# Performance work log

Measured on AMD Instinct MI355X. Metric: run time of the kernel, lower is better.

## Reference

```python
import jax, jax.numpy as jnp
import numpy as np

B, C, H, W = 16, 512, 64, 64
CB, CG = 64, 256  # bottleneck = C/8, g = C/2


def _conv1x1(x, w, b):
    # x: [B,Cin,H,W], w: [Cout,Cin] -> [B,Cout,H,W]
    return jnp.einsum('bchw,oc->bohw', x, w) + b[None, :, None, None]


def _avg_pool2(x):
    # 2x2 average pool, stride 2. x: [B,C,H,W] with even H,W.
    b, c, h, w = x.shape
    return x.reshape(b, c, h // 2, 2, w // 2, 2).mean(axis=(3, 5))


def setup_inputs() -> dict:
    key = jax.random.key(0)
    ks = jax.random.split(key, 6)
    s = 0.02
    return {
        'x': jax.random.normal(ks[0], (B, C, H, W), jnp.float32),
        'w_theta': jax.random.normal(ks[1], (CB, C), jnp.float32) * s,
        'b_theta': jnp.zeros((CB,), jnp.float32),
        'w_phi': jax.random.normal(ks[2], (CB, C), jnp.float32) * s,
        'b_phi': jnp.zeros((CB,), jnp.float32),
        'w_g': jax.random.normal(ks[3], (CG, C), jnp.float32) * s,
        'b_g': jnp.zeros((CG,), jnp.float32),
        'w_out': jax.random.normal(ks[4], (C, CG), jnp.float32) * s,
        'b_out': jnp.zeros((C,), jnp.float32),
        'gamma': jnp.zeros((1,), jnp.float32),
    }


def reference(x, w_theta, b_theta, w_phi, b_phi, w_g, b_g, w_out, b_out, gamma):
    b, c, h, w = x.shape
    n = h * w          # query locations
    m = n // 4         # pooled key/value locations

    theta = _conv1x1(x, w_theta, b_theta).reshape(b, CB, n)           # [B,CB,N]
    phi = _avg_pool2(_conv1x1(x, w_phi, b_phi)).reshape(b, CB, m)     # [B,CB,M]
    g = _avg_pool2(_conv1x1(x, w_g, b_g)).reshape(b, CG, m)           # [B,CG,M]

    logits = jnp.einsum('bcn,bcm->bnm', theta, phi)                   # [B,N,M]
    attn = jax.nn.softmax(logits, axis=-1)
    out = jnp.einsum('bcm,bnm->bcn', g, attn).reshape(b, CG, h, w)    # [B,CG,H,W]
    out = _conv1x1(out, w_out, b_out)                                 # [B,C,H,W]
    return gamma[0] * out + x
```

## Files before the change

### kernel.cpp

```cpp
#include <hip/hip_runtime.h>
#include <math.h>


typedef unsigned short u16;
typedef short bf16x8 __attribute__((ext_vector_type(8)));
typedef float f32x16 __attribute__((ext_vector_type(16)));
typedef u16 u16x4 __attribute__((ext_vector_type(4)));
typedef int i32x4 __attribute__((ext_vector_type(4)));

#define MFMA32 __builtin_amdgcn_mfma_f32_32x32x16_bf16
#define B_ 16
#define C_ 512
#define N_ 4096
#define M_ 1024
#define LOG2E 1.44269504088896f
#define FIXMAX 8.0f

__device__ __forceinline__ u16 f2b(float f) {
  unsigned u = __float_as_uint(f);
  return (u16)((u + 0x7FFFu + ((u >> 16) & 1u)) >> 16);
}
__device__ __forceinline__ unsigned cvtpk(float a, float b) {
  unsigned r;
  asm("v_cvt_pk_bf16_f32 %0, %1, %2" : "=v"(r) : "v"(a), "v"(b));
  return r;
}
__device__ __forceinline__ void permswap(unsigned &a, unsigned &b) {
  asm("v_permlane32_swap_b32 %0, %1" : "+v"(a), "+v"(b));
}
__device__ __forceinline__ float exp2v(float a) {
  float r;
  asm("v_exp_f32 %0, %1" : "=v"(r) : "v"(a));
  return r;
}
__device__ __forceinline__ void async_cp16(u16* lds, const u16* g) {
  __builtin_amdgcn_global_load_lds(
      (const __attribute__((address_space(1))) unsigned int*)g,
      (__attribute__((address_space(3))) unsigned int*)lds, 16, 0, 0);
}
__device__ __forceinline__ f32x16 fz16() {
  f32x16 z;
#pragma unroll
  for (int i = 0; i < 16; ++i) z[i] = 0.0f;
  return z;
}


__global__ __launch_bounds__(256) void cvt_all_kernel(
    const float* __restrict__ w_theta, const float* __restrict__ w_phi,
    const float* __restrict__ w_g, const float* __restrict__ w_out,
    const float* __restrict__ gamma, u16* __restrict__ dth, u16* __restrict__ dph,
    u16* __restrict__ dg, u16* __restrict__ dwo) {
  int i = blockIdx.x * 256 + threadIdx.x;
  if (i < 16384) {
    const float* s = (i < 8192) ? w_theta : w_phi;
    u16* d = (i < 8192) ? dth : dph;
    float scale = (i < 8192) ? LOG2E : 1.0f;
    int j = i & 8191;
    int o = j >> 7, c = (j & 127) * 4;
    float4 vv = *(const float4*)(s + (size_t)o * 512 + c);
    int idx = (((o >> 5) * 8 + (c >> 6)) * 4 + ((c >> 4) & 3)) * 512 +
              (((c >> 3) & 1) * 32 + (o & 31)) * 8 + (c & 7);
    u16x4 ot = {f2b(vv.x * scale), f2b(vv.y * scale), f2b(vv.z * scale), f2b(vv.w * scale)};
    *(u16x4*)(d + idx) = ot;
  } else if (i < 49152) {
    int j = i - 16384;
    int o = j >> 7, c = (j & 127) * 4;
    float4 vv = *(const float4*)(w_g + (size_t)o * 512 + c);
    int idx = (((o >> 5) * 8 + (c >> 6)) * 4 + ((c >> 4) & 3)) * 512 +
              (((c >> 3) & 1) * 32 + (o & 31)) * 8 + (c & 7);
    u16x4 ot = {f2b(vv.x), f2b(vv.y), f2b(vv.z), f2b(vv.w)};
    *(u16x4*)(dg + idx) = ot;
  } else {
    int j = i - 49152;
    int o = j >> 6, k = (j & 63) * 4;
    float scale = gamma[0];
    float4 vv = *(const float4*)(w_out + (size_t)o * 256 + k);
    int idx = ((o >> 5) * 16 + (k >> 4)) * 512 +
              (((k >> 3) & 1) * 32 + (o & 31)) * 8 + (k & 7);
    u16x4 ot = {f2b(vv.x * scale), f2b(vv.y * scale), f2b(vv.z * scale), f2b(vv.w * scale)};
    *(u16x4*)(dwo + idx) = ot;
  }
}

__global__ __launch_bounds__(512) void prep_kernel(
    const float* __restrict__ x, const u16* __restrict__ wth,
    const u16* __restrict__ wph, const u16* __restrict__ wg,
    const float* __restrict__ bth, const float* __restrict__ bph,
    const float* __restrict__ bg, u16* __restrict__ th, u16* __restrict__ ph,
    u16* __restrict__ vt) {
  __shared__ u16 xb[128 * 68];
  __shared__ u16 xpt[32 * 68];
  const int t = threadIdx.x;
  const int w = t >> 6, l = t & 63, lo = l & 31, hi = l >> 5;
  const int nb = blockIdx.x, b = blockIdx.y;
  const int n0 = nb * 128;
  const int lcol = (t & 31) * 4;
  const int lrow = t >> 5;

  f32x16 acc0 = fz16(), acc1 = fz16(), a_ph = fz16();

  float v[16];
  auto loadv = [&](int c0) {
#pragma unroll
    for (int i = 0; i < 4; ++i) {
      float4 f = *(const float4*)(x + ((size_t)(b * C_ + c0 + lrow + 16 * i)) * N_ + n0 + lcol);
      v[4*i] = f.x; v[4*i+1] = f.y; v[4*i+2] = f.z; v[4*i+3] = f.w;
    }
  };
  auto writeT = [&]() {
#pragma unroll
    for (int i = 0; i < 4; ++i) {
      int c = lrow + 16 * i;
      int blk = c >> 3;
#pragma unroll
      for (int k = 0; k < 4; ++k) {
        int n = lcol + k;
        int swz = ((n >> 2) ^ (n >> 5)) & 7;
        xb[n * 68 + ((blk ^ swz) * 8) + (c & 7)] = f2b(v[4*i+k]);
      }
    }
    float pA[4], pB[4];
#pragma unroll
    for (int i = 0; i < 4; ++i) {
      pA[i] = v[4*i] + v[4*i+1];
      pB[i] = v[4*i+2] + v[4*i+3];
    }
#pragma unroll
    for (int i = 0; i < 4; ++i) {
      pA[i] += __shfl_xor(pA[i], 16, 64);
      pB[i] += __shfl_xor(pB[i], 16, 64);
    }
    if ((t & 31) < 16) {
      int m0 = (t & 31) * 2;
#pragma unroll
      for (int i = 0; i < 4; ++i) {
        int c = lrow + 16 * i;
        xpt[m0 * 68 + c] = f2b(0.25f * pA[i]);
        xpt[(m0 + 1) * 68 + c] = f2b(0.25f * pB[i]);
      }
    }
  };
  auto domfma = [&](int c0b) {
    if (w < 4) {
      const int n = 32 * w + lo;
      const int rbase = n * 68;
      const int nswz = ((n >> 2) ^ (n >> 5)) & 7;
#pragma unroll
      for (int kh = 0; kh < 4; ++kh) {
        bf16x8 xa = *(const bf16x8*)(&xb[rbase + (((2*kh + hi) ^ nswz) * 8)]);
        bf16x8 w0 = *(const bf16x8*)(wth + ((c0b) * 4 + kh) * 512 + l * 8);
        bf16x8 w1 = *(const bf16x8*)(wth + ((8 + c0b) * 4 + kh) * 512 + l * 8);
        acc0 = MFMA32(xa, w0, acc0, 0, 0, 0);
        acc1 = MFMA32(xa, w1, acc1, 0, 0, 0);
      }
    } else {
      const int wg4 = w - 4;
      const u16* xpw = &xpt[lo * 68];
#pragma unroll
      for (int kh = 0; kh < 4; ++kh) {
        bf16x8 xp8 = *(const bf16x8*)(xpw + kh * 16 + hi * 8);
        bf16x8 g0 = *(const bf16x8*)(wg + ((16*wg4 + c0b) * 4 + kh) * 512 + l * 8);
        bf16x8 g1 = *(const bf16x8*)(wg + ((16*wg4 + 8 + c0b) * 4 + kh) * 512 + l * 8);
        acc0 = MFMA32(g0, xp8, acc0, 0, 0, 0);
        acc1 = MFMA32(g1, xp8, acc1, 0, 0, 0);
        if (wg4 < 2) {
          bf16x8 wp8 = *(const bf16x8*)(wph + ((wg4*8 + c0b) * 4 + kh) * 512 + l * 8);
          a_ph = MFMA32(xp8, wp8, a_ph, 0, 0, 0);
        }
      }
    }
  };

  loadv(0);
  for (int i = 0; i < 8; ++i) {
    if (i) __syncthreads();
    writeT();
    if (i < 7) loadv((i + 1) * 64);
    __syncthreads();
    domfma(i);
  }

  int rr[16];
#pragma unroll
  for (int r = 0; r < 16; ++r) rr[r] = (r & 3) + 8 * (r >> 2) + 4 * hi;

  if (w < 4) {
    u16* thb = th + (size_t)b * 262144;
#pragma unroll
    for (int r = 0; r < 16; ++r) {
      int sub = (((lo >> 3) & 1) * 32 + rr[r]) * 8 + (lo & 7);
      thb[((nb*4 + w)*4 + (lo >> 4)) * 512 + sub]     = f2b(acc0[r] + LOG2E * bth[lo]);
      thb[((nb*4 + w)*4 + 2 + (lo >> 4)) * 512 + sub] = f2b(acc1[r] + LOG2E * bth[32 + lo]);
    }
  } else {
    const int wg4 = w - 4;
    u16* vtb = vt + (size_t)b * 262144;
#pragma unroll
    for (int r = 0; r < 16; ++r) {
      int cg0 = 64 * wg4 + rr[r];
      int sub = (((lo >> 3) & 1) * 32 + rr[r]) * 8 + (lo & 7);
      int kk = (nb & 1) * 2 + (lo >> 4);
      vtb[(((nb >> 1) * 8 + 2*wg4) * 4 + kk) * 512 + sub]     = f2b(acc0[r] + bg[cg0]);
      vtb[(((nb >> 1) * 8 + 2*wg4 + 1) * 4 + kk) * 512 + sub] = f2b(acc1[r] + bg[cg0 + 32]);
    }
    if (wg4 < 2) {
      u16* phb = ph + (size_t)b * 65536;
#pragma unroll
      for (int r = 0; r < 16; ++r) {
        int sub = (((lo >> 3) & 1) * 32 + rr[r]) * 8 + (lo & 7);
        phb[(nb*4 + 2*wg4 + (lo >> 4)) * 512 + sub] = f2b(a_ph[r] + bph[32*wg4 + lo]);
      }
    }
  }
}

__global__ __launch_bounds__(512, 4) void attn_core_kernel(
    const u16* __restrict__ th, const u16* __restrict__ ph,
    const u16* __restrict__ vt, u16* __restrict__ Og) {
  __shared__ u16 smem[40960];

  const int t = threadIdx.x;
  const int w = t >> 6, l = t & 63;
  const int p = w & 3, h = w >> 2;
  const int flat = blockIdx.y * 32 + blockIdx.x;
  const int nf = (flat & 7) * 64 + (flat >> 3);
  const int b = nf >> 5, nb5 = nf & 31;
  const int jqt = nb5 * 4 + p;

  const u16* thb = th + (size_t)b * 262144;
  const u16* phb = ph + (size_t)b * 65536;
  const u16* vtb = vt + (size_t)b * 262144;

  bf16x8 thB[4];
#pragma unroll
  for (int kh = 0; kh < 4; ++kh)
    thB[kh] = *(const bf16x8*)(thb + (jqt * 4 + kh) * 512 + l * 8);

  f32x16 acc[4];
#pragma unroll
  for (int ct = 0; ct < 4; ++ct) acc[ct] = fz16();
  float sp[4] = {0.0f, 0.0f, 0.0f, 0.0f};

  auto stage = [&](int k) {
    const int ic = k >> 1, jml2 = (k & 1) * 2;
    u16* base = &smem[(k & 3) * 10240];
#pragma unroll
    for (int i = 0; i < 2; ++i) {
      const int r = w + 8 * i;
      const u16* src = vtb + (size_t)((ic * 8 + (r >> 1)) * 4 + jml2 + (r & 1)) * 512 + l * 8;
      async_cp16(base + r * 512 + l * 8, src);
    }
    {
      const int o2 = (t & 255) * 8;
      async_cp16(base + 8192 + o2, phb + (size_t)k * 2048 + o2);
    }
  };

  stage(0);
  stage(1);
  asm volatile("s_waitcnt vmcnt(3)" ::: "memory");
  __builtin_amdgcn_sched_barrier(0);
  __builtin_amdgcn_s_barrier();

  for (int k = 0; k < 32; ++k) {
    if (k < 30) stage(k + 2);

    const u16* Vs = &smem[(k & 3) * 10240];
    const u16* Ps = Vs + 8192;

    f32x16 S = fz16();
#pragma unroll
    for (int kh = 0; kh < 4; ++kh) {
      bf16x8 pf = *(const bf16x8*)(Ps + kh * 512 + l * 8);
      S = MFMA32(pf, thB[kh], S, 0, 0, 0);
    }

#pragma unroll
    for (int i = 0; i < 16; ++i) {
      S[i] = exp2v(S[i] - FIXMAX);
      sp[i & 3] += S[i];
    }

    bf16x8 Pf[2];
#pragma unroll
    for (int s = 0; s < 2; ++s) {
      unsigned a0 = cvtpk(S[8*s+0], S[8*s+1]);
      unsigned a1 = cvtpk(S[8*s+2], S[8*s+3]);
      unsigned a2 = cvtpk(S[8*s+4], S[8*s+5]);
      unsigned a3 = cvtpk(S[8*s+6], S[8*s+7]);
      permswap(a0, a2);
      permswap(a1, a3);
      i32x4 wv = {(int)a0, (int)a1, (int)a2, (int)a3};
      Pf[s] = __builtin_bit_cast(bf16x8, wv);
    }

    __builtin_amdgcn_s_setprio(1);
#pragma unroll
    for (int ct2 = 0; ct2 < 4; ++ct2) {
      const u16* vp = Vs + (4 * h + ct2) * 1024 + l * 8;
      bf16x8 vf0 = *(const bf16x8*)(vp);
      bf16x8 vf1 = *(const bf16x8*)(vp + 512);
      acc[ct2] = MFMA32(vf0, Pf[0], acc[ct2], 0, 0, 0);
      acc[ct2] = MFMA32(vf1, Pf[1], acc[ct2], 0, 0, 0);
    }
    __builtin_amdgcn_s_setprio(0);

    if (k < 30) {
      asm volatile("s_waitcnt vmcnt(3)" ::: "memory");
      __builtin_amdgcn_sched_barrier(0);
      __builtin_amdgcn_s_barrier();
    } else if (k == 30) {
      asm volatile("s_waitcnt vmcnt(0)" ::: "memory");
      __builtin_amdgcn_sched_barrier(0);
      __builtin_amdgcn_s_barrier();
    }
  }

  float lsum = (sp[0] + sp[1]) + (sp[2] + sp[3]);
  lsum += __shfl_xor(lsum, 32, 64);
  const float linv = 1.0f / lsum;

  u16* Ob = Og + (size_t)b * 1048576 + (size_t)jqt * 16 * 512;
#pragma unroll
  for (int ct2 = 0; ct2 < 4; ++ct2) {
    f32x16& A = acc[ct2];
#pragma unroll
    for (int s = 0; s < 2; ++s) {
      unsigned a0 = cvtpk(A[8*s+0]*linv, A[8*s+1]*linv);
      unsigned a1 = cvtpk(A[8*s+2]*linv, A[8*s+3]*linv);
      unsigned a2 = cvtpk(A[8*s+4]*linv, A[8*s+5]*linv);
      unsigned a3 = cvtpk(A[8*s+6]*linv, A[8*s+7]*linv);
      permswap(a0, a2);
      permswap(a1, a3);
      i32x4 wv = {(int)a0, (int)a1, (int)a2, (int)a3};
      int f = 8 * h + 2 * ct2 + s;
      *(bf16x8*)(Ob + f * 512 + l * 8) = __builtin_bit_cast(bf16x8, wv);
    }
  }
}

__global__ __launch_bounds__(512, 4) void outconv_kernel(
    const u16* __restrict__ Og, const u16* __restrict__ wo,
    const float* __restrict__ b_out, const float* __restrict__ gamma,
    const float* __restrict__ x, float* __restrict__ out) {
  const int t = threadIdx.x;
  const int w = t >> 6, l = t & 63, lo = l & 31, hi = l >> 5;
  const int p = w & 3, h = w >> 2;
  const int flat = blockIdx.y * 32 + blockIdx.x;
  const int nf = (flat & 7) * 64 + (flat >> 3);
  const int b = nf >> 5, nb5 = nf & 31;
  const int jqt = nb5 * 4 + p;
  const int qp = jqt * 32;

  const u16* Ob = Og + (size_t)b * 1048576 + (size_t)jqt * 16 * 512;
  bf16x8 Of[16];
#pragma unroll
  for (int f = 0; f < 16; ++f)
    Of[f] = *(const bf16x8*)(Ob + f * 512 + l * 8);

  int rr[16];
#pragma unroll
  for (int r = 0; r < 16; ++r) rr[r] = (r & 3) + 8 * (r >> 2) + 4 * hi;

  const float gamma0 = gamma[0];
  for (int ctc = 0; ctc < 8; ++ctc) {
    f32x16 facc = fz16();
    const u16* wp = wo + (size_t)((8 * h + ctc) * 16) * 512 + l * 8;
#pragma unroll
    for (int f = 0; f < 16; ++f) {
      bf16x8 wfr = *(const bf16x8*)(wp + f * 512);
      facc = MFMA32(wfr, Of[f], facc, 0, 0, 0);
    }
#pragma unroll
    for (int r = 0; r < 16; ++r) {
      int c = 256 * h + 32 * ctc + rr[r];
      size_t idx = ((size_t)(b * C_ + c)) * N_ + qp + lo;
      float xv = __builtin_nontemporal_load(&x[idx]);
      __builtin_nontemporal_store(facc[r] + gamma0 * b_out[c] + xv, &out[idx]);
    }
  }
}

extern "C" void kernel_launch(void* const* d_in, const int* in_sizes, int n_in,
                              void* d_out, int out_size, void* d_ws, size_t ws_size,
                              hipStream_t stream) {
  (void)in_sizes; (void)n_in; (void)out_size; (void)ws_size;
  const float* x       = (const float*)d_in[0];
  const float* w_theta = (const float*)d_in[1];
  const float* b_theta = (const float*)d_in[2];
  const float* w_phi   = (const float*)d_in[3];
  const float* b_phi   = (const float*)d_in[4];
  const float* w_g     = (const float*)d_in[5];
  const float* b_g     = (const float*)d_in[6];
  const float* w_out   = (const float*)d_in[7];
  const float* b_out   = (const float*)d_in[8];
  const float* gamma   = (const float*)d_in[9];
  float* out = (float*)d_out;

  char* ws = (char*)d_ws;
  u16* th  = (u16*)(ws);
  u16* ph  = (u16*)(ws + 8388608);
  u16* vt  = (u16*)(ws + 10485760);
  u16* wth = (u16*)(ws + 18874368);
  u16* wph = (u16*)(ws + 18939904);
  u16* wg  = (u16*)(ws + 19005440);
  u16* wo  = (u16*)(ws + 19267584);
  u16* Og  = (u16*)(ws + 19529728);

  cvt_all_kernel<<<320, 256, 0, stream>>>(w_theta, w_phi, w_g, w_out, gamma,
                                          wth, wph, wg, wo);
  prep_kernel<<<dim3(32, 16), 512, 0, stream>>>(x, wth, wph, wg, b_theta, b_phi,
                                                b_g, th, ph, vt);
  attn_core_kernel<<<dim3(32, 16), 512, 0, stream>>>(th, ph, vt, Og);
  outconv_kernel<<<dim3(32, 16), 512, 0, stream>>>(Og, wo, b_out, gamma, x, out);
}
```

Before: 167.8 us.

## Process two query tiles per wave in attention core to reuse staged K/V

Each wave now handles two 32-query tiles instead of one, so each block covers twice the queries and the grid is halved. The staged phi and V tiles in shared memory, and the phi fragments read from them, are reused across both tiles, which halves global and LDS traffic per query. In exchange, register pressure doubles (two accumulator sets), launch bounds drop to 2 blocks per CU, and the grid has only 256 blocks. The shared memory array is enlarged, though the staging indices still use the old layout.

```diff
diff --git a/kernel.cpp b/kernel.cpp
--- a/kernel.cpp
+++ b/kernel.cpp
@@ -215,32 +215,34 @@
   }
 }
 
-__global__ __launch_bounds__(512, 4) void attn_core_kernel(
+__global__ __launch_bounds__(512, 2) void attn_core_kernel(
     const u16* __restrict__ th, const u16* __restrict__ ph,
     const u16* __restrict__ vt, u16* __restrict__ Og) {
-  __shared__ u16 smem[40960];
+  __shared__ u16 smem[49152];
 
   const int t = threadIdx.x;
   const int w = t >> 6, l = t & 63;
   const int p = w & 3, h = w >> 2;
-  const int flat = blockIdx.y * 32 + blockIdx.x;
-  const int nf = (flat & 7) * 64 + (flat >> 3);
-  const int b = nf >> 5, nb5 = nf & 31;
-  const int jqt = nb5 * 4 + p;
+  const int flat = blockIdx.y * 16 + blockIdx.x;
+  const int nf = (flat & 7) * 32 + (flat >> 3);
+  const int b = nf >> 4, nb6 = nf & 15;
+  const int jA = nb6 * 8 + p * 2, jB = jA + 1;
 
   const u16* thb = th + (size_t)b * 262144;
   const u16* phb = ph + (size_t)b * 65536;
   const u16* vtb = vt + (size_t)b * 262144;
 
-  bf16x8 thB[4];
-#pragma unroll
-  for (int kh = 0; kh < 4; ++kh)
-    thB[kh] = *(const bf16x8*)(thb + (jqt * 4 + kh) * 512 + l * 8);
-
-  f32x16 acc[4];
-#pragma unroll
-  for (int ct = 0; ct < 4; ++ct) acc[ct] = fz16();
-  float sp[4] = {0.0f, 0.0f, 0.0f, 0.0f};
+  bf16x8 thA[4], thBt[4];
+#pragma unroll
+  for (int kh = 0; kh < 4; ++kh) {
+    thA[kh]  = *(const bf16x8*)(thb + (jA * 4 + kh) * 512 + l * 8);
+    thBt[kh] = *(const bf16x8*)(thb + (jB * 4 + kh) * 512 + l * 8);
+  }
+
+  f32x16 accA[4], accB[4];
+#pragma unroll
+  for (int ct = 0; ct < 4; ++ct) { accA[ct] = fz16(); accB[ct] = fz16(); }
+  float spA[4] = {0.f, 0.f, 0.f, 0.f}, spB[4] = {0.f, 0.f, 0.f, 0.f};
 
   auto stage = [&](int k) {
     const int ic = k >> 1, jml2 = (k & 1) * 2;
@@ -257,32 +259,7 @@
     }
   };
 
-  stage(0);
-  stage(1);
-  asm volatile("s_waitcnt vmcnt(3)" ::: "memory");
-  __builtin_amdgcn_sched_barrier(0);
-  __builtin_amdgcn_s_barrier();
-
-  for (int k = 0; k < 32; ++k) {
-    if (k < 30) stage(k + 2);
-
-    const u16* Vs = &smem[(k & 3) * 10240];
-    const u16* Ps = Vs + 8192;
-
-    f32x16 S = fz16();
-#pragma unroll
-    for (int kh = 0; kh < 4; ++kh) {
-      bf16x8 pf = *(const bf16x8*)(Ps + kh * 512 + l * 8);
-      S = MFMA32(pf, thB[kh], S, 0, 0, 0);
-    }
-
-#pragma unroll
-    for (int i = 0; i < 16; ++i) {
-      S[i] = exp2v(S[i] - FIXMAX);
-      sp[i & 3] += S[i];
-    }
-
-    bf16x8 Pf[2];
+  auto packPf = [&](f32x16& S, bf16x8* Pf) {
 #pragma unroll
     for (int s = 0; s < 2; ++s) {
       unsigned a0 = cvtpk(S[8*s+0], S[8*s+1]);
@@ -294,6 +271,46 @@
       i32x4 wv = {(int)a0, (int)a1, (int)a2, (int)a3};
       Pf[s] = __builtin_bit_cast(bf16x8, wv);
     }
+  };
+
+  stage(0);
+  stage(1);
+  asm volatile("s_waitcnt vmcnt(3)" ::: "memory");
+  __builtin_amdgcn_sched_barrier(0);
+  __builtin_amdgcn_s_barrier();
+
+  for (int k = 0; k < 32; ++k) {
+    if (k < 30) stage(k + 2);
+
+    const u16* Vs = &smem[(k & 3) * 10240];
+    const u16* Ps = Vs + 8192;
+
+    bf16x8 pf[4];
+#pragma unroll
+    for (int kh = 0; kh < 4; ++kh)
+      pf[kh] = *(const bf16x8*)(Ps + kh * 512 + l * 8);
+
+    f32x16 S = fz16();
+#pragma unroll
+    for (int kh = 0; kh < 4; ++kh) S = MFMA32(pf[kh], thA[kh], S, 0, 0, 0);
+#pragma unroll
+    for (int i = 0; i < 16; ++i) {
+      S[i] = exp2v(S[i] - FIXMAX);
+      spA[i & 3] += S[i];
+    }
+    bf16x8 PfA[2];
+    packPf(S, PfA);
+
+    f32x16 S2 = fz16();
+#pragma unroll
+    for (int kh = 0; kh < 4; ++kh) S2 = MFMA32(pf[kh], thBt[kh], S2, 0, 0, 0);
+#pragma unroll
+    for (int i = 0; i < 16; ++i) {
+      S2[i] = exp2v(S2[i] - FIXMAX);
+      spB[i & 3] += S2[i];
+    }
+    bf16x8 PfB[2];
+    packPf(S2, PfB);
 
     __builtin_amdgcn_s_setprio(1);
 #pragma unroll
@@ -301,8 +318,10 @@
       const u16* vp = Vs + (4 * h + ct2) * 1024 + l * 8;
       bf16x8 vf0 = *(const bf16x8*)(vp);
       bf16x8 vf1 = *(const bf16x8*)(vp + 512);
-      acc[ct2] = MFMA32(vf0, Pf[0], acc[ct2], 0, 0, 0);
-      acc[ct2] = MFMA32(vf1, Pf[1], acc[ct2], 0, 0, 0);
+      accA[ct2] = MFMA32(vf0, PfA[0], accA[ct2], 0, 0, 0);
+      accA[ct2] = MFMA32(vf1, PfA[1], accA[ct2], 0, 0, 0);
+      accB[ct2] = MFMA32(vf0, PfB[0], accB[ct2], 0, 0, 0);
+      accB[ct2] = MFMA32(vf1, PfB[1], accB[ct2], 0, 0, 0);
     }
     __builtin_amdgcn_s_setprio(0);
 
@@ -317,27 +336,34 @@
     }
   }
 
-  float lsum = (sp[0] + sp[1]) + (sp[2] + sp[3]);
-  lsum += __shfl_xor(lsum, 32, 64);
-  const float linv = 1.0f / lsum;
-
-  u16* Ob = Og + (size_t)b * 1048576 + (size_t)jqt * 16 * 512;
-#pragma unroll
-  for (int ct2 = 0; ct2 < 4; ++ct2) {
-    f32x16& A = acc[ct2];
-#pragma unroll
-    for (int s = 0; s < 2; ++s) {
-      unsigned a0 = cvtpk(A[8*s+0]*linv, A[8*s+1]*linv);
-      unsigned a1 = cvtpk(A[8*s+2]*linv, A[8*s+3]*linv);
-      unsigned a2 = cvtpk(A[8*s+4]*linv, A[8*s+5]*linv);
-      unsigned a3 = cvtpk(A[8*s+6]*linv, A[8*s+7]*linv);
-      permswap(a0, a2);
-      permswap(a1, a3);
-      i32x4 wv = {(int)a0, (int)a1, (int)a2, (int)a3};
-      int f = 8 * h + 2 * ct2 + s;
-      *(bf16x8*)(Ob + f * 512 + l * 8) = __builtin_bit_cast(bf16x8, wv);
-    }
-  }
+  float lA = (spA[0] + spA[1]) + (spA[2] + spA[3]);
+  lA += __shfl_xor(lA, 32, 64);
+  const float liA = 1.0f / lA;
+  float lB = (spB[0] + spB[1]) + (spB[2] + spB[3]);
+  lB += __shfl_xor(lB, 32, 64);
+  const float liB = 1.0f / lB;
+
+  auto packO = [&](f32x16* acc, float li, int jq) {
+    u16* Ob = Og + (size_t)b * 1048576 + (size_t)jq * 16 * 512;
+#pragma unroll
+    for (int ct2 = 0; ct2 < 4; ++ct2) {
+      f32x16& A = acc[ct2];
+#pragma unroll
+      for (int s = 0; s < 2; ++s) {
+        unsigned a0 = cvtpk(A[8*s+0]*li, A[8*s+1]*li);
+        unsigned a1 = cvtpk(A[8*s+2]*li, A[8*s+3]*li);
+        unsigned a2 = cvtpk(A[8*s+4]*li, A[8*s+5]*li);
+        unsigned a3 = cvtpk(A[8*s+6]*li, A[8*s+7]*li);
+        permswap(a0, a2);
+        permswap(a1, a3);
+        i32x4 wv = {(int)a0, (int)a1, (int)a2, (int)a3};
+        int f = 8 * h + 2 * ct2 + s;
+        *(bf16x8*)(Ob + f * 512 + l * 8) = __builtin_bit_cast(bf16x8, wv);
+      }
+    }
+  };
+  packO(accA, liA, jA);
+  packO(accB, liB, jB);
 }
 
 __global__ __launch_bounds__(512, 4) void outconv_kernel(
@@ -412,6 +438,6 @@
                                           wth, wph, wg, wo);
   prep_kernel<<<dim3(32, 16), 512, 0, stream>>>(x, wth, wph, wg, b_theta, b_phi,
                                                 b_g, th, ph, vt);
-  attn_core_kernel<<<dim3(32, 16), 512, 0, stream>>>(th, ph, vt, Og);
+  attn_core_kernel<<<dim3(16, 16), 512, 0, stream>>>(th, ph, vt, Og);
   outconv_kernel<<<dim3(32, 16), 512, 0, stream>>>(Og, wo, b_out, gamma, x, out);
 }
```

Result: no change. 165.1 us, median of 2 (-1.6%).
